# Optimization experiments

Hardware: AMD Instinct MI355X
Metric: run time of the kernel (lower is better)

## Reference

```python
import jax, jax.numpy as jnp
import numpy as np

T, D, H, P, HEADS, EC = 16, 192, 128, 128, 4, 32  # EC = proj_dim // 4
HD = P // HEADS  # head dim = 32


def setup_inputs() -> dict:
    key = jax.random.key(0)
    ks = jax.random.split(key, 16)
    def nrm(k, shp, s=0.02):
        return jax.random.normal(k, shp, jnp.float32) * s
    x = jax.random.normal(ks[0], (T, H, D), jnp.float32)
    u = jax.random.uniform(ks[1], (D, D))
    w = jax.random.uniform(ks[2], (D, D))
    edge_w = jnp.where(u < 0.05, w, 0.0)
    return dict(
        x=x, edge_w=edge_w,
        W_node=nrm(ks[3], (H, P)), b_node=jnp.zeros(P),
        W_edge=nrm(ks[4], (1, EC)), b_edge=jnp.zeros(EC),
        time_enc=nrm(ks[5], (P,)),
        Wqkv=nrm(ks[6], (P, 3 * P)), bqkv=jnp.zeros(3 * P),
        Wo=nrm(ks[7], (P, P)), bo=jnp.zeros(P),
        W1=nrm(ks[8], (P, 4 * P)), b1=jnp.zeros(4 * P),
        W2=nrm(ks[9], (4 * P, P)), b2=jnp.zeros(P),
        g1=jnp.ones(P), beta1=jnp.zeros(P), g2=jnp.ones(P), beta2=jnp.zeros(P),
        Wc1=nrm(ks[10], (2 * P + EC, P)), bc1=jnp.zeros(P),
        Wc2=nrm(ks[11], (P, 1)), bc2=jnp.zeros(1),
        Wd1=nrm(ks[12], (2 * P, P)), bd1=jnp.zeros(P),
        Wd2=nrm(ks[13], (P, 1)), bd2=jnp.zeros(1),
    )


def _ln(z, g, b):
    m = z.mean(-1, keepdims=True)
    v = ((z - m) ** 2).mean(-1, keepdims=True)
    return (z - m) / jnp.sqrt(v + 1e-5) * g + b


def _heads(t, S):
    return t.reshape(S, HEADS, HD).transpose(1, 0, 2)  # (h, S, hd)


def _forward(x, edge_w, W_node, b_node, W_edge, b_edge, time_enc, Wqkv, bqkv,
             Wo, bo, W1, b1, W2, b2, g1, beta1, g2, beta2,
             Wc1, bc1, Wc2, bc2, Wd1, bd1, Wd2, bd2):
    S = T * D
    # node encoder: (T,H,D) -> (T,D,H) -> (T*D,H) -> (T*D,P), dropout is eval-mode identity
    xf = x.transpose(0, 2, 1).reshape(S, H)
    h = jax.nn.relu(xf @ W_node + b_node)
    # learned time encoding scaled by time index
    t_idx = jnp.repeat(jnp.arange(T, dtype=jnp.float32), D)
    h = h + time_enc[None, :] * t_idx[:, None]
    # spatiotemporal mask: attend to self+neighbors at t and t-1 (vectorized kron)
    adj = (edge_w > 0) | jnp.eye(D, dtype=bool)
    time_allow = jnp.eye(T, dtype=bool) | jnp.eye(T, k=-1, dtype=bool)
    allow = (time_allow[:, None, :, None] & adj[None, :, None, :]).reshape(S, S)
    scale = 1.0 / np.sqrt(HD)
    z = h
    for _ in range(2):  # num_layers=2, shared weights as in the source
        y = _ln(z, g1, beta1)
        qkv = y @ Wqkv + bqkv
        q, k, v = jnp.split(qkv, 3, axis=-1)
        scores = jnp.einsum('hqd,hkd->hqk', _heads(q, S), _heads(k, S)) * scale
        scores = jnp.where(allow[None], scores, -jnp.inf)
        a = jax.nn.softmax(scores, axis=-1)
        attn = jnp.einsum('hqk,hkd->hqd', a, _heads(v, S))
        z = z + attn.transpose(1, 0, 2).reshape(S, P) @ Wo + bo
        y = _ln(z, g2, beta2)
        z = z + jax.nn.relu(y @ W1 + b1) @ W2 + b2
    nf = z.reshape(T, D, P)
    curr, nxt = nf[:-1], nf[1:]  # (T-1, D, P)
    # edge encoder: Linear(1->EC)+ReLU on edge weights
    edge_enc = jax.nn.relu(edge_w[:, :, None] * W_edge[0] + b_edge)  # (D, D, EC)
    # update classifier on concat[next_i, curr_j, edge] -> split the first matmul
    hn = nxt @ Wc1[:P]            # (T-1, D, P)
    hc = curr @ Wc1[P:2 * P]      # (T-1, D, P)
    he = edge_enc @ Wc1[2 * P:]   # (D, D, P)
    hcls = jax.nn.relu(hn[:, :, None, :] + hc[:, None, :, :] + he[None] + bc1)
    logits = (hcls @ Wc2)[..., 0] + bc2[0]  # (T-1, D, D)
    mask = (edge_w == 0) & ~jnp.eye(D, dtype=bool)
    logits = jnp.where(mask[None], -1e9, logits)
    # distance predictor on concat[curr, next]
    hd = jax.nn.relu(curr @ Wd1[:P] + nxt @ Wd1[P:] + bd1)
    dist = (hd @ Wd2)[..., 0] + bd2[0]  # (T-1, D)
    return logits, dist


def reference(x, edge_w, W_node, b_node, W_edge, b_edge, time_enc, Wqkv, bqkv,
              Wo, bo, W1, b1, W2, b2, g1, beta1, g2, beta2,
              Wc1, bc1, Wc2, bc2, Wd1, bd1, Wd2, bd2):
    return _forward(x, edge_w, W_node, b_node, W_edge, b_edge, time_enc, Wqkv,
                    bqkv, Wo, bo, W1, b1, W2, b2, g1, beta1, g2, beta2,
                    Wc1, bc1, Wc2, bc2, Wd1, bd1, Wd2, bd2)
```

## Files before the change

kernel.cpp:

```cpp
#include <hip/hip_runtime.h>

constexpr int T_ = 16;
constexpr int D_ = 192;
constexpr int H_ = 128;
constexpr int P_ = 128;
constexpr int EC_ = 32;
constexpr int S_ = T_ * D_;
constexpr int FF_ = 512;
constexpr float SCALE_ = 0.17677669529663687f;

__device__ __forceinline__ float wave_sum64(float v) {
#pragma unroll
  for (int m = 1; m < 64; m <<= 1) v += __shfl_xor(v, m);
  return v;
}

__global__ __launch_bounds__(128) void embed_adj_kernel(
    const float* __restrict__ x, const float* __restrict__ W_node,
    const float* __restrict__ b_node, const float* __restrict__ time_enc,
    const float* __restrict__ edge_w, float* __restrict__ z,
    int* __restrict__ adj_cnt, int* __restrict__ adj_list) {
  int bx = blockIdx.x;
  int tid = threadIdx.x;
  if (bx < D_ && tid < 64) {
    int lane = tid, cnt = 0;
    for (int base = 0; base < D_; base += 64) {
      int j = base + lane;
      bool pred = (edge_w[bx * D_ + j] > 0.f) || (j == bx);
      unsigned long long mb = __ballot(pred);
      int ofs = __popcll(mb & ((1ull << lane) - 1ull));
      if (pred) adj_list[bx * D_ + cnt + ofs] = j;
      cnt += __popcll(mb);
    }
    if (lane == 0) adj_cnt[bx] = cnt;
  }
  __shared__ float As[8 * H_];
  int m0 = bx * 8;
  for (int idx = tid; idx < 8 * H_; idx += 128) {
    int r = idx >> 7, h = idx & 127;
    int s = m0 + r, t = s / D_, d = s - t * D_;
    As[idx] = x[(t * H_ + h) * D_ + d];
  }
  __syncthreads();
  int j = tid;
  float acc[8];
  float bj = b_node[j];
#pragma unroll
  for (int r = 0; r < 8; ++r) acc[r] = bj;
  for (int h = 0; h < H_; h += 4) {
    float w0 = W_node[(h + 0) * P_ + j], w1 = W_node[(h + 1) * P_ + j];
    float w2 = W_node[(h + 2) * P_ + j], w3 = W_node[(h + 3) * P_ + j];
#pragma unroll
    for (int r = 0; r < 8; ++r) {
      const float4 a = *reinterpret_cast<const float4*>(&As[r * H_ + h]);
      acc[r] = fmaf(a.x, w0, acc[r]);
      acc[r] = fmaf(a.y, w1, acc[r]);
      acc[r] = fmaf(a.z, w2, acc[r]);
      acc[r] = fmaf(a.w, w3, acc[r]);
    }
  }
  float te = time_enc[j];
#pragma unroll
  for (int r = 0; r < 8; ++r) {
    int s = m0 + r;
    z[(size_t)s * P_ + j] = fmaxf(acc[r], 0.f) + te * (float)(s / D_);
  }
}

__global__ __launch_bounds__(192) void qkv_kernel(
    const float* __restrict__ z, const float* __restrict__ Wqkv,
    const float* __restrict__ bqkv, const float* __restrict__ g,
    const float* __restrict__ b, float* __restrict__ qkvb) {
  constexpr int BM = 16, NT = 192, N = 384;
  int m0 = blockIdx.x * BM;
  int tid = threadIdx.x;
  __shared__ float As[BM * 128];
  {
    float4* As4 = (float4*)As;
    const float4* Z4 = (const float4*)(z + (size_t)m0 * 128);
    for (int idx = tid; idx < BM * 32; idx += NT) As4[idx] = Z4[idx];
  }
  __syncthreads();
  {
    int wv = tid >> 6, lane = tid & 63;
    for (int r = wv; r < BM; r += 3) {
      float v0 = As[r * 128 + lane], v1 = As[r * 128 + 64 + lane];
      float s = wave_sum64(v0 + v1);
      float mean = s * (1.f / 128.f);
      float d0 = v0 - mean, d1 = v1 - mean;
      float q = wave_sum64(d0 * d0 + d1 * d1);
      float inv = 1.f / sqrtf(q * (1.f / 128.f) + 1e-5f);
      As[r * 128 + lane] = d0 * inv * g[lane] + b[lane];
      As[r * 128 + 64 + lane] = d1 * inv * g[lane + 64] + b[lane + 64];
    }
  }
  __syncthreads();
  int c0 = 2 * tid;
  float acc0[BM], acc1[BM];
  float b0c = bqkv[c0], b1c = bqkv[c0 + 1];
#pragma unroll
  for (int r = 0; r < BM; ++r) {
    acc0[r] = b0c;
    acc1[r] = b1c;
  }
  for (int k = 0; k < 128; k += 4) {
    float2 bv0 = *(const float2*)(Wqkv + (size_t)(k + 0) * N + c0);
    float2 bv1 = *(const float2*)(Wqkv + (size_t)(k + 1) * N + c0);
    float2 bv2 = *(const float2*)(Wqkv + (size_t)(k + 2) * N + c0);
    float2 bv3 = *(const float2*)(Wqkv + (size_t)(k + 3) * N + c0);
#pragma unroll
    for (int r = 0; r < BM; ++r) {
      const float4 a = *(const float4*)&As[r * 128 + k];
      acc0[r] = fmaf(a.x, bv0.x, acc0[r]);
      acc1[r] = fmaf(a.x, bv0.y, acc1[r]);
      acc0[r] = fmaf(a.y, bv1.x, acc0[r]);
      acc1[r] = fmaf(a.y, bv1.y, acc1[r]);
      acc0[r] = fmaf(a.z, bv2.x, acc0[r]);
      acc1[r] = fmaf(a.z, bv2.y, acc1[r]);
      acc0[r] = fmaf(a.w, bv3.x, acc0[r]);
      acc1[r] = fmaf(a.w, bv3.y, acc1[r]);
    }
  }
#pragma unroll
  for (int r = 0; r < BM; ++r) {
    float2 nv;
    nv.x = acc0[r];
    nv.y = acc1[r];
    *(float2*)(qkvb + (size_t)(m0 + r) * N + c0) = nv;
  }
}

__global__ __launch_bounds__(128) void attn_wo_kernel(
    const float* __restrict__ qkvb, const int* __restrict__ adj_cnt,
    const int* __restrict__ adj_list, const float* __restrict__ Wo,
    const float* __restrict__ bo, float* __restrict__ z) {
  int s = blockIdx.x;
  int t = s / D_, d1 = s - t * D_;
  int tid = threadIdx.x;
  __shared__ int klist[D_];
  __shared__ float scores[4][2 * D_];
  __shared__ float att[128];

  int nd2 = adj_cnt[d1];
  for (int kd = tid; kd < nd2; kd += 128) klist[kd] = adj_list[d1 * D_ + kd];
  __syncthreads();
  int t0 = (t > 0) ? t - 1 : 0;
  int ntp = (t > 0) ? 2 : 1;
  int nk = nd2 * ntp;

  float q = qkvb[(size_t)s * 384 + tid];
  int h = tid >> 5, dd = tid & 31;

  for (int tp = 0; tp < ntp; ++tp) {
    int tt = t0 + tp;
    for (int kd = 0; kd < nd2; ++kd) {
      int sk = tt * D_ + klist[kd];
      float partial = q * qkvb[(size_t)sk * 384 + P_ + tid];
      partial += __shfl_xor(partial, 1);
      partial += __shfl_xor(partial, 2);
      partial += __shfl_xor(partial, 4);
      partial += __shfl_xor(partial, 8);
      partial += __shfl_xor(partial, 16);
      if (dd == 0) scores[h][tp * nd2 + kd] = partial * SCALE_;
    }
  }
  float mx = -1e30f;
  for (int ki = dd; ki < nk; ki += 32) mx = fmaxf(mx, scores[h][ki]);
  mx = fmaxf(mx, __shfl_xor(mx, 1));
  mx = fmaxf(mx, __shfl_xor(mx, 2));
  mx = fmaxf(mx, __shfl_xor(mx, 4));
  mx = fmaxf(mx, __shfl_xor(mx, 8));
  mx = fmaxf(mx, __shfl_xor(mx, 16));
  float ssum = 0.f;
  for (int ki = dd; ki < nk; ki += 32) {
    float e = expf(scores[h][ki] - mx);
    scores[h][ki] = e;
    ssum += e;
  }
  ssum += __shfl_xor(ssum, 1);
  ssum += __shfl_xor(ssum, 2);
  ssum += __shfl_xor(ssum, 4);
  ssum += __shfl_xor(ssum, 8);
  ssum += __shfl_xor(ssum, 16);
  float inv = 1.f / ssum;

  float acc = 0.f;
  for (int tp = 0; tp < ntp; ++tp) {
    int tt = t0 + tp;
    for (int kd = 0; kd < nd2; ++kd) {
      float aev = scores[h][tp * nd2 + kd];
      int sk = tt * D_ + klist[kd];
      acc = fmaf(aev, qkvb[(size_t)sk * 384 + 2 * P_ + tid], acc);
    }
  }
  att[tid] = acc * inv;
  __syncthreads();

  int c = tid;
  float p = 0.f;
  for (int k = 0; k < 128; k += 4) {
    const float4 a = *(const float4*)&att[k];
    p = fmaf(a.x, Wo[(size_t)(k + 0) * P_ + c], p);
    p = fmaf(a.y, Wo[(size_t)(k + 1) * P_ + c], p);
    p = fmaf(a.z, Wo[(size_t)(k + 2) * P_ + c], p);
    p = fmaf(a.w, Wo[(size_t)(k + 3) * P_ + c], p);
  }
  z[(size_t)s * P_ + c] += p + bo[c];
}

__global__ __launch_bounds__(256) void ffn_kernel(
    const float* __restrict__ zin, const float* __restrict__ W1,
    const float* __restrict__ b1, const float* __restrict__ W2,
    const float* __restrict__ b2, const float* __restrict__ g,
    const float* __restrict__ b, float* __restrict__ z) {
  constexpr int BM = 8, NT = 256;
  int m0 = blockIdx.x * BM;
  int tid = threadIdx.x;
  __shared__ float As[BM * 128];
  __shared__ float mid[BM * FF_];
  {
    float4* As4 = (float4*)As;
    const float4* Z4 = (const float4*)(zin + (size_t)m0 * 128);
    for (int idx = tid; idx < BM * 32; idx += NT) As4[idx] = Z4[idx];
  }
  __syncthreads();
  {
    int wv = tid >> 6, lane = tid & 63;
    for (int r = wv; r < BM; r += 4) {
      float v0 = As[r * 128 + lane], v1 = As[r * 128 + 64 + lane];
      float s = wave_sum64(v0 + v1);
      float mean = s * (1.f / 128.f);
      float d0 = v0 - mean, d1 = v1 - mean;
      float qv = wave_sum64(d0 * d0 + d1 * d1);
      float inv = 1.f / sqrtf(qv * (1.f / 128.f) + 1e-5f);
      As[r * 128 + lane] = d0 * inv * g[lane] + b[lane];
      As[r * 128 + 64 + lane] = d1 * inv * g[lane + 64] + b[lane + 64];
    }
  }
  __syncthreads();
  {
    int c0 = 2 * tid;
    float acc0[BM], acc1[BM];
    float bb0 = b1[c0], bb1 = b1[c0 + 1];
#pragma unroll
    for (int r = 0; r < BM; ++r) {
      acc0[r] = bb0;
      acc1[r] = bb1;
    }
    for (int k = 0; k < 128; k += 4) {
      float2 bv0 = *(const float2*)(W1 + (size_t)(k + 0) * FF_ + c0);
      float2 bv1 = *(const float2*)(W1 + (size_t)(k + 1) * FF_ + c0);
      float2 bv2 = *(const float2*)(W1 + (size_t)(k + 2) * FF_ + c0);
      float2 bv3 = *(const float2*)(W1 + (size_t)(k + 3) * FF_ + c0);
#pragma unroll
      for (int r = 0; r < BM; ++r) {
        const float4 a = *(const float4*)&As[r * 128 + k];
        acc0[r] = fmaf(a.x, bv0.x, acc0[r]);
        acc1[r] = fmaf(a.x, bv0.y, acc1[r]);
        acc0[r] = fmaf(a.y, bv1.x, acc0[r]);
        acc1[r] = fmaf(a.y, bv1.y, acc1[r]);
        acc0[r] = fmaf(a.z, bv2.x, acc0[r]);
        acc1[r] = fmaf(a.z, bv2.y, acc1[r]);
        acc0[r] = fmaf(a.w, bv3.x, acc0[r]);
        acc1[r] = fmaf(a.w, bv3.y, acc1[r]);
      }
    }
#pragma unroll
    for (int r = 0; r < BM; ++r) {
      mid[r * FF_ + c0] = fmaxf(acc0[r], 0.f);
      mid[r * FF_ + c0 + 1] = fmaxf(acc1[r], 0.f);
    }
  }
  __syncthreads();
  {
    int rg = tid >> 7, col = tid & 127;
    int r0 = rg * 4;
    float acc[4] = {0.f, 0.f, 0.f, 0.f};
    for (int k = 0; k < FF_; k += 4) {
      float w0 = W2[(size_t)(k + 0) * P_ + col];
      float w1 = W2[(size_t)(k + 1) * P_ + col];
      float w2 = W2[(size_t)(k + 2) * P_ + col];
      float w3 = W2[(size_t)(k + 3) * P_ + col];
#pragma unroll
      for (int i = 0; i < 4; ++i) {
        const float4 a = *(const float4*)&mid[(r0 + i) * FF_ + k];
        acc[i] = fmaf(a.x, w0, acc[i]);
        acc[i] = fmaf(a.y, w1, acc[i]);
        acc[i] = fmaf(a.z, w2, acc[i]);
        acc[i] = fmaf(a.w, w3, acc[i]);
      }
    }
    float bb = b2[col];
#pragma unroll
    for (int i = 0; i < 4; ++i)
      z[(size_t)(m0 + r0 + i) * P_ + col] += acc[i] + bb;
  }
}

__global__ __launch_bounds__(256) void pre_gemm_kernel(
    const float* __restrict__ A, const float* __restrict__ Wc1,
    const float* __restrict__ Wd1, float* __restrict__ pre) {
  constexpr int K = 128, N = 512, NT = 256, BM = 8;
  int m0 = blockIdx.x * BM;
  int tid = threadIdx.x;
  __shared__ float As[BM * K];
  {
    float4* As4 = (float4*)As;
    const float4* A4 = (const float4*)(A + (size_t)m0 * K);
    for (int idx = tid; idx < BM * K / 4; idx += NT) As4[idx] = A4[idx];
  }
  __syncthreads();
  int c0 = 2 * tid;
  int seg = c0 >> 7, cc = c0 & 127;
  const float* Bbase = (seg < 2 ? Wc1 : Wd1) + ((seg & 1) ? P_ * P_ : 0) + cc;
  float acc0[BM], acc1[BM];
#pragma unroll
  for (int r = 0; r < BM; ++r) {
    acc0[r] = 0.f;
    acc1[r] = 0.f;
  }
  for (int k = 0; k < K; k += 4) {
    float2 bv0 = *(const float2*)(Bbase + (size_t)(k + 0) * P_);
    float2 bv1 = *(const float2*)(Bbase + (size_t)(k + 1) * P_);
    float2 bv2 = *(const float2*)(Bbase + (size_t)(k + 2) * P_);
    float2 bv3 = *(const float2*)(Bbase + (size_t)(k + 3) * P_);
#pragma unroll
    for (int r = 0; r < BM; ++r) {
      const float4 a = *(const float4*)&As[r * K + k];
      acc0[r] = fmaf(a.x, bv0.x, acc0[r]);
      acc1[r] = fmaf(a.x, bv0.y, acc1[r]);
      acc0[r] = fmaf(a.y, bv1.x, acc0[r]);
      acc1[r] = fmaf(a.y, bv1.y, acc1[r]);
      acc0[r] = fmaf(a.z, bv2.x, acc0[r]);
      acc1[r] = fmaf(a.z, bv2.y, acc1[r]);
      acc0[r] = fmaf(a.w, bv3.x, acc0[r]);
      acc1[r] = fmaf(a.w, bv3.y, acc1[r]);
    }
  }
#pragma unroll
  for (int r = 0; r < BM; ++r) {
    float2 nv;
    nv.x = acc0[r];
    nv.y = acc1[r];
    *(float2*)(pre + (size_t)(m0 + r) * N + c0) = nv;
  }
}

__global__ __launch_bounds__(64) void logits_dist_kernel(
    const float* __restrict__ pre, const int* __restrict__ adj_cnt,
    const int* __restrict__ adj_list, const float* __restrict__ edge_w,
    const float* __restrict__ W_edge, const float* __restrict__ b_edge,
    const float* __restrict__ Wc1e, const float* __restrict__ bc1,
    const float* __restrict__ Wc2, const float* __restrict__ bc2,
    const float* __restrict__ bd1, const float* __restrict__ Wd2,
    const float* __restrict__ bd2, float* __restrict__ logits,
    float* __restrict__ dist) {
  int i = blockIdx.x;
  int t = blockIdx.y;
  int lane = threadIdx.x;
  int w = t * D_ + i;
  float* lrow = logits + (size_t)w * D_;
  for (int j = lane; j < D_; j += 64) lrow[j] = -1e9f;

  const float* hnr = pre + (size_t)((t + 1) * D_ + i) * 512;
  float hn0 = hnr[lane], hn1 = hnr[lane + 64];
  float bc1_0 = bc1[lane], bc1_1 = bc1[lane + 64];
  float wc0 = Wc2[lane], wc1 = Wc2[lane + 64];
  float bb = bc2[0];
  int cnt = adj_cnt[i];
  for (int jj = 0; jj < cnt; ++jj) {
    int j = adj_list[i * D_ + jj];
    float wv = edge_w[i * D_ + j];
    float he0 = 0.f, he1 = 0.f;
#pragma unroll 8
    for (int e = 0; e < EC_; ++e) {
      float enc = fmaxf(fmaf(wv, W_edge[e], b_edge[e]), 0.f);
      he0 = fmaf(enc, Wc1e[e * P_ + lane], he0);
      he1 = fmaf(enc, Wc1e[e * P_ + lane + 64], he1);
    }
    const float* hcr = pre + (size_t)(t * D_ + j) * 512 + 128;
    float sacc = fmaxf(hn0 + hcr[lane] + he0 + bc1_0, 0.f) * wc0 +
                 fmaxf(hn1 + hcr[lane + 64] + he1 + bc1_1, 0.f) * wc1;
    sacc = wave_sum64(sacc);
    if (lane == 0) lrow[j] = sacc + bb;
  }

  const float* ar = pre + (size_t)w * 512 + 256;
  const float* br = pre + (size_t)(w + D_) * 512 + 384;
  float v0 = fmaxf(ar[lane] + br[lane] + bd1[lane], 0.f) * Wd2[lane];
  float v1 = fmaxf(ar[lane + 64] + br[lane + 64] + bd1[lane + 64], 0.f) * Wd2[lane + 64];
  float sd = wave_sum64(v0 + v1);
  if (lane == 0) dist[w] = sd + bd2[0];
}

extern "C" void kernel_launch(void* const* d_in, const int* in_sizes, int n_in,
                              void* d_out, int out_size, void* d_ws,
                              size_t ws_size, hipStream_t stream) {
  const float* x = (const float*)d_in[0];
  const float* edge_w = (const float*)d_in[1];
  const float* W_node = (const float*)d_in[2];
  const float* b_node = (const float*)d_in[3];
  const float* W_edge = (const float*)d_in[4];
  const float* b_edge = (const float*)d_in[5];
  const float* time_enc = (const float*)d_in[6];
  const float* Wqkv = (const float*)d_in[7];
  const float* bqkv = (const float*)d_in[8];
  const float* Wo = (const float*)d_in[9];
  const float* bo = (const float*)d_in[10];
  const float* W1 = (const float*)d_in[11];
  const float* b1 = (const float*)d_in[12];
  const float* W2 = (const float*)d_in[13];
  const float* b2 = (const float*)d_in[14];
  const float* g1 = (const float*)d_in[15];
  const float* beta1 = (const float*)d_in[16];
  const float* g2 = (const float*)d_in[17];
  const float* beta2 = (const float*)d_in[18];
  const float* Wc1 = (const float*)d_in[19];
  const float* bc1 = (const float*)d_in[20];
  const float* Wc2 = (const float*)d_in[21];
  const float* bc2 = (const float*)d_in[22];
  const float* Wd1 = (const float*)d_in[23];
  const float* bd1 = (const float*)d_in[24];
  const float* Wd2 = (const float*)d_in[25];
  const float* bd2 = (const float*)d_in[26];

  float* ws = (float*)d_ws;
  float* z = ws;
  float* qkvb = z + S_ * 128;
  float* pre = qkvb + S_ * 384;
  int* adj_cnt = (int*)(pre + S_ * 512);
  int* adj_list = adj_cnt + D_;

  float* logits = (float*)d_out;
  float* dist = (float*)d_out + (T_ - 1) * D_ * D_;

  embed_adj_kernel<<<S_ / 8, 128, 0, stream>>>(x, W_node, b_node, time_enc,
                                               edge_w, z, adj_cnt, adj_list);
  for (int it = 0; it < 2; ++it) {
    qkv_kernel<<<S_ / 16, 192, 0, stream>>>(z, Wqkv, bqkv, g1, beta1, qkvb);
    attn_wo_kernel<<<S_, 128, 0, stream>>>(qkvb, adj_cnt, adj_list, Wo, bo, z);
    ffn_kernel<<<S_ / 8, 256, 0, stream>>>(z, W1, b1, W2, b2, g2, beta2, z);
  }
  pre_gemm_kernel<<<S_ / 8, 256, 0, stream>>>(z, Wc1, Wd1, pre);
  logits_dist_kernel<<<dim3(D_, T_ - 1), 64, 0, stream>>>(
      pre, adj_cnt, adj_list, edge_w, W_edge, b_edge, Wc1 + 2 * P_ * P_, bc1,
      Wc2, bc2, bd1, Wd2, bd2, logits, dist);
}
```

Baseline: 326.1 us.

## Fuse attention, output projection and FFN into one tail kernel; widen GEMM blocks

Merges the per-row attention+Wo kernel and the FFN kernel into a single 512-thread tail kernel. Each block handles 8 rows: four 128-thread groups compute attention for two rows each, then the Wo projection, LayerNorm, and both FFN GEMMs run on data kept in shared memory. This removes one launch per layer and a global round-trip of z. The qkv and pre-GEMM kernels are also reshaped to one output column per thread with more threads and fewer rows per block. In exchange, the attention part now runs fewer blocks with extra barriers, and the smaller row tiles reuse each weight load less.

```diff
diff --git a/kernel.cpp b/kernel.cpp
--- a/kernel.cpp
+++ b/kernel.cpp
@@ -67,23 +67,23 @@
   }
 }
 
-__global__ __launch_bounds__(192) void qkv_kernel(
+__global__ __launch_bounds__(384) void qkv_kernel(
     const float* __restrict__ z, const float* __restrict__ Wqkv,
     const float* __restrict__ bqkv, const float* __restrict__ g,
     const float* __restrict__ b, float* __restrict__ qkvb) {
-  constexpr int BM = 16, NT = 192, N = 384;
+  constexpr int BM = 8, N = 384;
   int m0 = blockIdx.x * BM;
   int tid = threadIdx.x;
   __shared__ float As[BM * 128];
   {
     float4* As4 = (float4*)As;
     const float4* Z4 = (const float4*)(z + (size_t)m0 * 128);
-    for (int idx = tid; idx < BM * 32; idx += NT) As4[idx] = Z4[idx];
+    if (tid < 256) As4[tid] = Z4[tid];
   }
   __syncthreads();
   {
     int wv = tid >> 6, lane = tid & 63;
-    for (int r = wv; r < BM; r += 3) {
+    for (int r = wv; r < BM; r += 6) {
       float v0 = As[r * 128 + lane], v1 = As[r * 128 + 64 + lane];
       float s = wave_sum64(v0 + v1);
       float mean = s * (1.f / 128.f);
@@ -95,255 +95,226 @@
     }
   }
   __syncthreads();
-  int c0 = 2 * tid;
-  float acc0[BM], acc1[BM];
-  float b0c = bqkv[c0], b1c = bqkv[c0 + 1];
-#pragma unroll
-  for (int r = 0; r < BM; ++r) {
-    acc0[r] = b0c;
-    acc1[r] = b1c;
-  }
+  int col = tid;
+  float acc[BM];
+  float bc = bqkv[col];
+#pragma unroll
+  for (int r = 0; r < BM; ++r) acc[r] = bc;
   for (int k = 0; k < 128; k += 4) {
-    float2 bv0 = *(const float2*)(Wqkv + (size_t)(k + 0) * N + c0);
-    float2 bv1 = *(const float2*)(Wqkv + (size_t)(k + 1) * N + c0);
-    float2 bv2 = *(const float2*)(Wqkv + (size_t)(k + 2) * N + c0);
-    float2 bv3 = *(const float2*)(Wqkv + (size_t)(k + 3) * N + c0);
+    float b0 = Wqkv[(size_t)(k + 0) * N + col];
+    float b1 = Wqkv[(size_t)(k + 1) * N + col];
+    float b2 = Wqkv[(size_t)(k + 2) * N + col];
+    float b3 = Wqkv[(size_t)(k + 3) * N + col];
 #pragma unroll
     for (int r = 0; r < BM; ++r) {
       const float4 a = *(const float4*)&As[r * 128 + k];
-      acc0[r] = fmaf(a.x, bv0.x, acc0[r]);
-      acc1[r] = fmaf(a.x, bv0.y, acc1[r]);
-      acc0[r] = fmaf(a.y, bv1.x, acc0[r]);
-      acc1[r] = fmaf(a.y, bv1.y, acc1[r]);
-      acc0[r] = fmaf(a.z, bv2.x, acc0[r]);
-      acc1[r] = fmaf(a.z, bv2.y, acc1[r]);
-      acc0[r] = fmaf(a.w, bv3.x, acc0[r]);
-      acc1[r] = fmaf(a.w, bv3.y, acc1[r]);
-    }
-  }
-#pragma unroll
-  for (int r = 0; r < BM; ++r) {
-    float2 nv;
-    nv.x = acc0[r];
-    nv.y = acc1[r];
-    *(float2*)(qkvb + (size_t)(m0 + r) * N + c0) = nv;
-  }
-}
-
-__global__ __launch_bounds__(128) void attn_wo_kernel(
+      acc[r] = fmaf(a.x, b0, acc[r]);
+      acc[r] = fmaf(a.y, b1, acc[r]);
+      acc[r] = fmaf(a.z, b2, acc[r]);
+      acc[r] = fmaf(a.w, b3, acc[r]);
+    }
+  }
+#pragma unroll
+  for (int r = 0; r < BM; ++r) qkvb[(size_t)(m0 + r) * N + col] = acc[r];
+}
+
+__global__ __launch_bounds__(512) void tail_kernel(
     const float* __restrict__ qkvb, const int* __restrict__ adj_cnt,
     const int* __restrict__ adj_list, const float* __restrict__ Wo,
-    const float* __restrict__ bo, float* __restrict__ z) {
-  int s = blockIdx.x;
-  int t = s / D_, d1 = s - t * D_;
-  int tid = threadIdx.x;
-  __shared__ int klist[D_];
-  __shared__ float scores[4][2 * D_];
-  __shared__ float att[128];
-
-  int nd2 = adj_cnt[d1];
-  for (int kd = tid; kd < nd2; kd += 128) klist[kd] = adj_list[d1 * D_ + kd];
-  __syncthreads();
-  int t0 = (t > 0) ? t - 1 : 0;
-  int ntp = (t > 0) ? 2 : 1;
-  int nk = nd2 * ntp;
-
-  float q = qkvb[(size_t)s * 384 + tid];
-  int h = tid >> 5, dd = tid & 31;
-
-  for (int tp = 0; tp < ntp; ++tp) {
-    int tt = t0 + tp;
-    for (int kd = 0; kd < nd2; ++kd) {
-      int sk = tt * D_ + klist[kd];
-      float partial = q * qkvb[(size_t)sk * 384 + P_ + tid];
-      partial += __shfl_xor(partial, 1);
-      partial += __shfl_xor(partial, 2);
-      partial += __shfl_xor(partial, 4);
-      partial += __shfl_xor(partial, 8);
-      partial += __shfl_xor(partial, 16);
-      if (dd == 0) scores[h][tp * nd2 + kd] = partial * SCALE_;
-    }
-  }
-  float mx = -1e30f;
-  for (int ki = dd; ki < nk; ki += 32) mx = fmaxf(mx, scores[h][ki]);
-  mx = fmaxf(mx, __shfl_xor(mx, 1));
-  mx = fmaxf(mx, __shfl_xor(mx, 2));
-  mx = fmaxf(mx, __shfl_xor(mx, 4));
-  mx = fmaxf(mx, __shfl_xor(mx, 8));
-  mx = fmaxf(mx, __shfl_xor(mx, 16));
-  float ssum = 0.f;
-  for (int ki = dd; ki < nk; ki += 32) {
-    float e = expf(scores[h][ki] - mx);
-    scores[h][ki] = e;
-    ssum += e;
-  }
-  ssum += __shfl_xor(ssum, 1);
-  ssum += __shfl_xor(ssum, 2);
-  ssum += __shfl_xor(ssum, 4);
-  ssum += __shfl_xor(ssum, 8);
-  ssum += __shfl_xor(ssum, 16);
-  float inv = 1.f / ssum;
-
-  float acc = 0.f;
-  for (int tp = 0; tp < ntp; ++tp) {
-    int tt = t0 + tp;
-    for (int kd = 0; kd < nd2; ++kd) {
-      float aev = scores[h][tp * nd2 + kd];
-      int sk = tt * D_ + klist[kd];
-      acc = fmaf(aev, qkvb[(size_t)sk * 384 + 2 * P_ + tid], acc);
-    }
-  }
-  att[tid] = acc * inv;
-  __syncthreads();
-
-  int c = tid;
-  float p = 0.f;
-  for (int k = 0; k < 128; k += 4) {
-    const float4 a = *(const float4*)&att[k];
-    p = fmaf(a.x, Wo[(size_t)(k + 0) * P_ + c], p);
-    p = fmaf(a.y, Wo[(size_t)(k + 1) * P_ + c], p);
-    p = fmaf(a.z, Wo[(size_t)(k + 2) * P_ + c], p);
-    p = fmaf(a.w, Wo[(size_t)(k + 3) * P_ + c], p);
-  }
-  z[(size_t)s * P_ + c] += p + bo[c];
-}
-
-__global__ __launch_bounds__(256) void ffn_kernel(
-    const float* __restrict__ zin, const float* __restrict__ W1,
+    const float* __restrict__ bo, const float* __restrict__ W1,
     const float* __restrict__ b1, const float* __restrict__ W2,
-    const float* __restrict__ b2, const float* __restrict__ g,
-    const float* __restrict__ b, float* __restrict__ z) {
-  constexpr int BM = 8, NT = 256;
+    const float* __restrict__ b2, const float* __restrict__ g2,
+    const float* __restrict__ beta2, float* __restrict__ z) {
+  constexpr int BM = 8;
   int m0 = blockIdx.x * BM;
   int tid = threadIdx.x;
-  __shared__ float As[BM * 128];
-  __shared__ float mid[BM * FF_];
-  {
-    float4* As4 = (float4*)As;
-    const float4* Z4 = (const float4*)(zin + (size_t)m0 * 128);
-    for (int idx = tid; idx < BM * 32; idx += NT) As4[idx] = Z4[idx];
-  }
-  __syncthreads();
+  __shared__ float att[BM][128];
+  __shared__ float zs[BM][128];
+  __shared__ __align__(16) unsigned char uA[32768];
+
+  {
+    int gq = tid >> 7, lt = tid & 127;
+    int h = lt >> 5, dd = lt & 31;
+    int* klist = (int*)(uA + gq * 8192);
+    float* scores = (float*)(uA + gq * 8192 + 768);
+    for (int qi = 0; qi < 2; ++qi) {
+      int r = gq * 2 + qi;
+      int s = m0 + r;
+      int t = s / D_, d1 = s - t * D_;
+      int nd2 = adj_cnt[d1];
+      __syncthreads();
+      for (int kd = lt; kd < nd2; kd += 128) klist[kd] = adj_list[d1 * D_ + kd];
+      __syncthreads();
+      int t0 = (t > 0) ? t - 1 : 0;
+      int ntp = (t > 0) ? 2 : 1;
+      int nk = nd2 * ntp;
+      float q = qkvb[(size_t)s * 384 + lt];
+      for (int tp = 0; tp < ntp; ++tp) {
+        int tt = t0 + tp;
+        for (int kd = 0; kd < nd2; ++kd) {
+          int sk = tt * D_ + klist[kd];
+          float partial = q * qkvb[(size_t)sk * 384 + P_ + lt];
+          partial += __shfl_xor(partial, 1);
+          partial += __shfl_xor(partial, 2);
+          partial += __shfl_xor(partial, 4);
+          partial += __shfl_xor(partial, 8);
+          partial += __shfl_xor(partial, 16);
+          if (dd == 0) scores[h * 384 + tp * nd2 + kd] = partial * SCALE_;
+        }
+      }
+      float mx = -1e30f;
+      for (int ki = dd; ki < nk; ki += 32) mx = fmaxf(mx, scores[h * 384 + ki]);
+      mx = fmaxf(mx, __shfl_xor(mx, 1));
+      mx = fmaxf(mx, __shfl_xor(mx, 2));
+      mx = fmaxf(mx, __shfl_xor(mx, 4));
+      mx = fmaxf(mx, __shfl_xor(mx, 8));
+      mx = fmaxf(mx, __shfl_xor(mx, 16));
+      float ssum = 0.f;
+      for (int ki = dd; ki < nk; ki += 32) {
+        float e = expf(scores[h * 384 + ki] - mx);
+        scores[h * 384 + ki] = e;
+        ssum += e;
+      }
+      ssum += __shfl_xor(ssum, 1);
+      ssum += __shfl_xor(ssum, 2);
+      ssum += __shfl_xor(ssum, 4);
+      ssum += __shfl_xor(ssum, 8);
+      ssum += __shfl_xor(ssum, 16);
+      float inv = 1.f / ssum;
+      float acc = 0.f;
+      for (int tp = 0; tp < ntp; ++tp) {
+        int tt = t0 + tp;
+        for (int kd = 0; kd < nd2; ++kd) {
+          float aev = scores[h * 384 + tp * nd2 + kd];
+          int sk = tt * D_ + klist[kd];
+          acc = fmaf(aev, qkvb[(size_t)sk * 384 + 2 * P_ + lt], acc);
+        }
+      }
+      att[r][lt] = acc * inv;
+    }
+  }
+  __syncthreads();
+
+  {
+    int col = tid & 127, rg = tid >> 7;
+    int r0 = rg * 2;
+    float p0 = 0.f, p1 = 0.f;
+    for (int k = 0; k < 128; k += 4) {
+      float w0 = Wo[(size_t)(k + 0) * P_ + col];
+      float w1 = Wo[(size_t)(k + 1) * P_ + col];
+      float w2 = Wo[(size_t)(k + 2) * P_ + col];
+      float w3 = Wo[(size_t)(k + 3) * P_ + col];
+      const float4 a0 = *(const float4*)&att[r0][k];
+      const float4 a1 = *(const float4*)&att[r0 + 1][k];
+      p0 = fmaf(a0.x, w0, p0); p0 = fmaf(a0.y, w1, p0);
+      p0 = fmaf(a0.z, w2, p0); p0 = fmaf(a0.w, w3, p0);
+      p1 = fmaf(a1.x, w0, p1); p1 = fmaf(a1.y, w1, p1);
+      p1 = fmaf(a1.z, w2, p1); p1 = fmaf(a1.w, w3, p1);
+    }
+    float bb = bo[col];
+    zs[r0][col] = z[(size_t)(m0 + r0) * P_ + col] + p0 + bb;
+    zs[r0 + 1][col] = z[(size_t)(m0 + r0 + 1) * P_ + col] + p1 + bb;
+  }
+  __syncthreads();
+
+  float* mid = (float*)uA;
+  float* ys = (float*)(uA + 16384);
+
   {
     int wv = tid >> 6, lane = tid & 63;
-    for (int r = wv; r < BM; r += 4) {
-      float v0 = As[r * 128 + lane], v1 = As[r * 128 + 64 + lane];
-      float s = wave_sum64(v0 + v1);
-      float mean = s * (1.f / 128.f);
-      float d0 = v0 - mean, d1 = v1 - mean;
-      float qv = wave_sum64(d0 * d0 + d1 * d1);
-      float inv = 1.f / sqrtf(qv * (1.f / 128.f) + 1e-5f);
-      As[r * 128 + lane] = d0 * inv * g[lane] + b[lane];
-      As[r * 128 + 64 + lane] = d1 * inv * g[lane + 64] + b[lane + 64];
-    }
-  }
-  __syncthreads();
-  {
-    int c0 = 2 * tid;
-    float acc0[BM], acc1[BM];
-    float bb0 = b1[c0], bb1 = b1[c0 + 1];
-#pragma unroll
-    for (int r = 0; r < BM; ++r) {
-      acc0[r] = bb0;
-      acc1[r] = bb1;
-    }
+    float v0 = zs[wv][lane], v1 = zs[wv][lane + 64];
+    float ssm = wave_sum64(v0 + v1);
+    float mean = ssm * (1.f / 128.f);
+    float d0 = v0 - mean, d1 = v1 - mean;
+    float qv = wave_sum64(d0 * d0 + d1 * d1);
+    float inv = 1.f / sqrtf(qv * (1.f / 128.f) + 1e-5f);
+    ys[wv * 128 + lane] = d0 * inv * g2[lane] + beta2[lane];
+    ys[wv * 128 + lane + 64] = d1 * inv * g2[lane + 64] + beta2[lane + 64];
+  }
+  __syncthreads();
+
+  {
+    int col = tid;
+    float acc[8];
+    float bb = b1[col];
+#pragma unroll
+    for (int r = 0; r < 8; ++r) acc[r] = bb;
     for (int k = 0; k < 128; k += 4) {
-      float2 bv0 = *(const float2*)(W1 + (size_t)(k + 0) * FF_ + c0);
-      float2 bv1 = *(const float2*)(W1 + (size_t)(k + 1) * FF_ + c0);
-      float2 bv2 = *(const float2*)(W1 + (size_t)(k + 2) * FF_ + c0);
-      float2 bv3 = *(const float2*)(W1 + (size_t)(k + 3) * FF_ + c0);
-#pragma unroll
-      for (int r = 0; r < BM; ++r) {
-        const float4 a = *(const float4*)&As[r * 128 + k];
-        acc0[r] = fmaf(a.x, bv0.x, acc0[r]);
-        acc1[r] = fmaf(a.x, bv0.y, acc1[r]);
-        acc0[r] = fmaf(a.y, bv1.x, acc0[r]);
-        acc1[r] = fmaf(a.y, bv1.y, acc1[r]);
-        acc0[r] = fmaf(a.z, bv2.x, acc0[r]);
-        acc1[r] = fmaf(a.z, bv2.y, acc1[r]);
-        acc0[r] = fmaf(a.w, bv3.x, acc0[r]);
-        acc1[r] = fmaf(a.w, bv3.y, acc1[r]);
+      float w0 = W1[(size_t)(k + 0) * FF_ + col];
+      float w1 = W1[(size_t)(k + 1) * FF_ + col];
+      float w2 = W1[(size_t)(k + 2) * FF_ + col];
+      float w3 = W1[(size_t)(k + 3) * FF_ + col];
+#pragma unroll
+      for (int r = 0; r < 8; ++r) {
+        const float4 a = *(const float4*)&ys[r * 128 + k];
+        acc[r] = fmaf(a.x, w0, acc[r]);
+        acc[r] = fmaf(a.y, w1, acc[r]);
+        acc[r] = fmaf(a.z, w2, acc[r]);
+        acc[r] = fmaf(a.w, w3, acc[r]);
       }
     }
 #pragma unroll
-    for (int r = 0; r < BM; ++r) {
-      mid[r * FF_ + c0] = fmaxf(acc0[r], 0.f);
-      mid[r * FF_ + c0 + 1] = fmaxf(acc1[r], 0.f);
-    }
-  }
-  __syncthreads();
-  {
-    int rg = tid >> 7, col = tid & 127;
-    int r0 = rg * 4;
-    float acc[4] = {0.f, 0.f, 0.f, 0.f};
+    for (int r = 0; r < 8; ++r) mid[r * FF_ + col] = fmaxf(acc[r], 0.f);
+  }
+  __syncthreads();
+
+  {
+    int col = tid & 127, rg = tid >> 7;
+    int r0 = rg * 2;
+    float a0 = 0.f, a1 = 0.f;
     for (int k = 0; k < FF_; k += 4) {
       float w0 = W2[(size_t)(k + 0) * P_ + col];
       float w1 = W2[(size_t)(k + 1) * P_ + col];
       float w2 = W2[(size_t)(k + 2) * P_ + col];
       float w3 = W2[(size_t)(k + 3) * P_ + col];
-#pragma unroll
-      for (int i = 0; i < 4; ++i) {
-        const float4 a = *(const float4*)&mid[(r0 + i) * FF_ + k];
-        acc[i] = fmaf(a.x, w0, acc[i]);
-        acc[i] = fmaf(a.y, w1, acc[i]);
-        acc[i] = fmaf(a.z, w2, acc[i]);
-        acc[i] = fmaf(a.w, w3, acc[i]);
-      }
+      const float4 m0v = *(const float4*)&mid[r0 * FF_ + k];
+      const float4 m1v = *(const float4*)&mid[(r0 + 1) * FF_ + k];
+      a0 = fmaf(m0v.x, w0, a0); a0 = fmaf(m0v.y, w1, a0);
+      a0 = fmaf(m0v.z, w2, a0); a0 = fmaf(m0v.w, w3, a0);
+      a1 = fmaf(m1v.x, w0, a1); a1 = fmaf(m1v.y, w1, a1);
+      a1 = fmaf(m1v.z, w2, a1); a1 = fmaf(m1v.w, w3, a1);
     }
     float bb = b2[col];
-#pragma unroll
-    for (int i = 0; i < 4; ++i)
-      z[(size_t)(m0 + r0 + i) * P_ + col] += acc[i] + bb;
-  }
-}
-
-__global__ __launch_bounds__(256) void pre_gemm_kernel(
+    z[(size_t)(m0 + r0) * P_ + col] = zs[r0][col] + a0 + bb;
+    z[(size_t)(m0 + r0 + 1) * P_ + col] = zs[r0 + 1][col] + a1 + bb;
+  }
+}
+
+__global__ __launch_bounds__(512) void pre_gemm_kernel(
     const float* __restrict__ A, const float* __restrict__ Wc1,
     const float* __restrict__ Wd1, float* __restrict__ pre) {
-  constexpr int K = 128, N = 512, NT = 256, BM = 8;
+  constexpr int K = 128, BM = 8;
   int m0 = blockIdx.x * BM;
   int tid = threadIdx.x;
   __shared__ float As[BM * K];
   {
     float4* As4 = (float4*)As;
     const float4* A4 = (const float4*)(A + (size_t)m0 * K);
-    for (int idx = tid; idx < BM * K / 4; idx += NT) As4[idx] = A4[idx];
-  }
-  __syncthreads();
-  int c0 = 2 * tid;
-  int seg = c0 >> 7, cc = c0 & 127;
+    if (tid < 256) As4[tid] = A4[tid];
+  }
+  __syncthreads();
+  int col = tid;
+  int seg = col >> 7, cc = col & 127;
   const float* Bbase = (seg < 2 ? Wc1 : Wd1) + ((seg & 1) ? P_ * P_ : 0) + cc;
-  float acc0[BM], acc1[BM];
-#pragma unroll
-  for (int r = 0; r < BM; ++r) {
-    acc0[r] = 0.f;
-    acc1[r] = 0.f;
-  }
+  float acc[BM];
+#pragma unroll
+  for (int r = 0; r < BM; ++r) acc[r] = 0.f;
   for (int k = 0; k < K; k += 4) {
-    float2 bv0 = *(const float2*)(Bbase + (size_t)(k + 0) * P_);
-    float2 bv1 = *(const float2*)(Bbase + (size_t)(k + 1) * P_);
-    float2 bv2 = *(const float2*)(Bbase + (size_t)(k + 2) * P_);
-    float2 bv3 = *(const float2*)(Bbase + (size_t)(k + 3) * P_);
+    float b0 = Bbase[(size_t)(k + 0) * P_];
+    float b1 = Bbase[(size_t)(k + 1) * P_];
+    float b2 = Bbase[(size_t)(k + 2) * P_];
+    float b3 = Bbase[(size_t)(k + 3) * P_];
 #pragma unroll
     for (int r = 0; r < BM; ++r) {
       const float4 a = *(const float4*)&As[r * K + k];
-      acc0[r] = fmaf(a.x, bv0.x, acc0[r]);
-      acc1[r] = fmaf(a.x, bv0.y, acc1[r]);
-      acc0[r] = fmaf(a.y, bv1.x, acc0[r]);
-      acc1[r] = fmaf(a.y, bv1.y, acc1[r]);
-      acc0[r] = fmaf(a.z, bv2.x, acc0[r]);
-      acc1[r] = fmaf(a.z, bv2.y, acc1[r]);
-      acc0[r] = fmaf(a.w, bv3.x, acc0[r]);
-      acc1[r] = fmaf(a.w, bv3.y, acc1[r]);
-    }
-  }
-#pragma unroll
-  for (int r = 0; r < BM; ++r) {
-    float2 nv;
-    nv.x = acc0[r];
-    nv.y = acc1[r];
-    *(float2*)(pre + (size_t)(m0 + r) * N + c0) = nv;
-  }
+      acc[r] = fmaf(a.x, b0, acc[r]);
+      acc[r] = fmaf(a.y, b1, acc[r]);
+      acc[r] = fmaf(a.z, b2, acc[r]);
+      acc[r] = fmaf(a.w, b3, acc[r]);
+    }
+  }
+#pragma unroll
+  for (int r = 0; r < BM; ++r) pre[(size_t)(m0 + r) * 512 + col] = acc[r];
 }
 
 __global__ __launch_bounds__(64) void logits_dist_kernel(
@@ -437,11 +408,11 @@
   embed_adj_kernel<<<S_ / 8, 128, 0, stream>>>(x, W_node, b_node, time_enc,
                                                edge_w, z, adj_cnt, adj_list);
   for (int it = 0; it < 2; ++it) {
-    qkv_kernel<<<S_ / 16, 192, 0, stream>>>(z, Wqkv, bqkv, g1, beta1, qkvb);
-    attn_wo_kernel<<<S_, 128, 0, stream>>>(qkvb, adj_cnt, adj_list, Wo, bo, z);
-    ffn_kernel<<<S_ / 8, 256, 0, stream>>>(z, W1, b1, W2, b2, g2, beta2, z);
-  }
-  pre_gemm_kernel<<<S_ / 8, 256, 0, stream>>>(z, Wc1, Wd1, pre);
+    qkv_kernel<<<S_ / 8, 384, 0, stream>>>(z, Wqkv, bqkv, g1, beta1, qkvb);
+    tail_kernel<<<S_ / 8, 512, 0, stream>>>(qkvb, adj_cnt, adj_list, Wo, bo,
+                                            W1, b1, W2, b2, g2, beta2, z);
+  }
+  pre_gemm_kernel<<<S_ / 8, 512, 0, stream>>>(z, Wc1, Wd1, pre);
   logits_dist_kernel<<<dim3(D_, T_ - 1), 64, 0, stream>>>(
       pre, adj_cnt, adj_list, edge_w, W_edge, b_edge, Wc1 + 2 * P_ * P_, bc1,
       Wc2, bc2, bd1, Wd2, bd2, logits, dist);
```

After: 334.5 us. +2.6%, slower.

## Shrink GEMM row tiles, widen blocks, and unroll attention key loops by two

Applied to the files above, without the earlier changes.

The row tiles of the embed, qkv and ffn kernels shrink to 4 rows. The qkv and pre_gemm kernels switch to one output column per thread, with 384 and 512 threads per block. This launches more and wider blocks so the compute units fill up better on the small problem, at the cost of loading each weight from global memory more times. The attention score and value loops are also unrolled by two, so independent loads and shuffle reductions can overlap and hide latency.

```diff
diff --git a/kernel.cpp b/kernel.cpp
--- a/kernel.cpp
+++ b/kernel.cpp
@@ -34,24 +34,24 @@
     }
     if (lane == 0) adj_cnt[bx] = cnt;
   }
-  __shared__ float As[8 * H_];
-  int m0 = bx * 8;
-  for (int idx = tid; idx < 8 * H_; idx += 128) {
+  __shared__ float As[4 * H_];
+  int m0 = bx * 4;
+  for (int idx = tid; idx < 4 * H_; idx += 128) {
     int r = idx >> 7, h = idx & 127;
     int s = m0 + r, t = s / D_, d = s - t * D_;
     As[idx] = x[(t * H_ + h) * D_ + d];
   }
   __syncthreads();
   int j = tid;
-  float acc[8];
+  float acc[4];
   float bj = b_node[j];
 #pragma unroll
-  for (int r = 0; r < 8; ++r) acc[r] = bj;
+  for (int r = 0; r < 4; ++r) acc[r] = bj;
   for (int h = 0; h < H_; h += 4) {
     float w0 = W_node[(h + 0) * P_ + j], w1 = W_node[(h + 1) * P_ + j];
     float w2 = W_node[(h + 2) * P_ + j], w3 = W_node[(h + 3) * P_ + j];
 #pragma unroll
-    for (int r = 0; r < 8; ++r) {
+    for (int r = 0; r < 4; ++r) {
       const float4 a = *reinterpret_cast<const float4*>(&As[r * H_ + h]);
       acc[r] = fmaf(a.x, w0, acc[r]);
       acc[r] = fmaf(a.y, w1, acc[r]);
@@ -61,29 +61,30 @@
   }
   float te = time_enc[j];
 #pragma unroll
-  for (int r = 0; r < 8; ++r) {
+  for (int r = 0; r < 4; ++r) {
     int s = m0 + r;
     z[(size_t)s * P_ + j] = fmaxf(acc[r], 0.f) + te * (float)(s / D_);
   }
 }
 
-__global__ __launch_bounds__(192) void qkv_kernel(
+__global__ __launch_bounds__(384) void qkv_kernel(
     const float* __restrict__ z, const float* __restrict__ Wqkv,
     const float* __restrict__ bqkv, const float* __restrict__ g,
     const float* __restrict__ b, float* __restrict__ qkvb) {
-  constexpr int BM = 16, NT = 192, N = 384;
+  constexpr int BM = 4, N = 384;
   int m0 = blockIdx.x * BM;
   int tid = threadIdx.x;
   __shared__ float As[BM * 128];
   {
     float4* As4 = (float4*)As;
     const float4* Z4 = (const float4*)(z + (size_t)m0 * 128);
-    for (int idx = tid; idx < BM * 32; idx += NT) As4[idx] = Z4[idx];
+    if (tid < BM * 32) As4[tid] = Z4[tid];
   }
   __syncthreads();
   {
     int wv = tid >> 6, lane = tid & 63;
-    for (int r = wv; r < BM; r += 3) {
+    if (wv < BM) {
+      int r = wv;
       float v0 = As[r * 128 + lane], v1 = As[r * 128 + 64 + lane];
       float s = wave_sum64(v0 + v1);
       float mean = s * (1.f / 128.f);
@@ -95,39 +96,27 @@
     }
   }
   __syncthreads();
-  int c0 = 2 * tid;
-  float acc0[BM], acc1[BM];
-  float b0c = bqkv[c0], b1c = bqkv[c0 + 1];
-#pragma unroll
-  for (int r = 0; r < BM; ++r) {
-    acc0[r] = b0c;
-    acc1[r] = b1c;
-  }
+  int col = tid;
+  float acc[BM];
+  float bc = bqkv[col];
+#pragma unroll
+  for (int r = 0; r < BM; ++r) acc[r] = bc;
   for (int k = 0; k < 128; k += 4) {
-    float2 bv0 = *(const float2*)(Wqkv + (size_t)(k + 0) * N + c0);
-    float2 bv1 = *(const float2*)(Wqkv + (size_t)(k + 1) * N + c0);
-    float2 bv2 = *(const float2*)(Wqkv + (size_t)(k + 2) * N + c0);
-    float2 bv3 = *(const float2*)(Wqkv + (size_t)(k + 3) * N + c0);
+    float b0 = Wqkv[(size_t)(k + 0) * N + col];
+    float b1 = Wqkv[(size_t)(k + 1) * N + col];
+    float b2 = Wqkv[(size_t)(k + 2) * N + col];
+    float b3 = Wqkv[(size_t)(k + 3) * N + col];
 #pragma unroll
     for (int r = 0; r < BM; ++r) {
       const float4 a = *(const float4*)&As[r * 128 + k];
-      acc0[r] = fmaf(a.x, bv0.x, acc0[r]);
-      acc1[r] = fmaf(a.x, bv0.y, acc1[r]);
-      acc0[r] = fmaf(a.y, bv1.x, acc0[r]);
-      acc1[r] = fmaf(a.y, bv1.y, acc1[r]);
-      acc0[r] = fmaf(a.z, bv2.x, acc0[r]);
-      acc1[r] = fmaf(a.z, bv2.y, acc1[r]);
-      acc0[r] = fmaf(a.w, bv3.x, acc0[r]);
-      acc1[r] = fmaf(a.w, bv3.y, acc1[r]);
-    }
-  }
-#pragma unroll
-  for (int r = 0; r < BM; ++r) {
-    float2 nv;
-    nv.x = acc0[r];
-    nv.y = acc1[r];
-    *(float2*)(qkvb + (size_t)(m0 + r) * N + c0) = nv;
-  }
+      acc[r] = fmaf(a.x, b0, acc[r]);
+      acc[r] = fmaf(a.y, b1, acc[r]);
+      acc[r] = fmaf(a.z, b2, acc[r]);
+      acc[r] = fmaf(a.w, b3, acc[r]);
+    }
+  }
+#pragma unroll
+  for (int r = 0; r < BM; ++r) qkvb[(size_t)(m0 + r) * N + col] = acc[r];
 }
 
 __global__ __launch_bounds__(128) void attn_wo_kernel(
@@ -153,44 +142,62 @@
 
   for (int tp = 0; tp < ntp; ++tp) {
     int tt = t0 + tp;
-    for (int kd = 0; kd < nd2; ++kd) {
+    int kd = 0;
+    for (; kd + 2 <= nd2; kd += 2) {
+      int sk0 = tt * D_ + klist[kd];
+      int sk1 = tt * D_ + klist[kd + 1];
+      float p0 = q * qkvb[(size_t)sk0 * 384 + P_ + tid];
+      float p1 = q * qkvb[(size_t)sk1 * 384 + P_ + tid];
+#pragma unroll
+      for (int m = 1; m < 32; m <<= 1) {
+        p0 += __shfl_xor(p0, m);
+        p1 += __shfl_xor(p1, m);
+      }
+      if (dd == 0) {
+        scores[h][tp * nd2 + kd] = p0 * SCALE_;
+        scores[h][tp * nd2 + kd + 1] = p1 * SCALE_;
+      }
+    }
+    if (kd < nd2) {
       int sk = tt * D_ + klist[kd];
-      float partial = q * qkvb[(size_t)sk * 384 + P_ + tid];
-      partial += __shfl_xor(partial, 1);
-      partial += __shfl_xor(partial, 2);
-      partial += __shfl_xor(partial, 4);
-      partial += __shfl_xor(partial, 8);
-      partial += __shfl_xor(partial, 16);
-      if (dd == 0) scores[h][tp * nd2 + kd] = partial * SCALE_;
+      float p = q * qkvb[(size_t)sk * 384 + P_ + tid];
+#pragma unroll
+      for (int m = 1; m < 32; m <<= 1) p += __shfl_xor(p, m);
+      if (dd == 0) scores[h][tp * nd2 + kd] = p * SCALE_;
     }
   }
   float mx = -1e30f;
   for (int ki = dd; ki < nk; ki += 32) mx = fmaxf(mx, scores[h][ki]);
-  mx = fmaxf(mx, __shfl_xor(mx, 1));
-  mx = fmaxf(mx, __shfl_xor(mx, 2));
-  mx = fmaxf(mx, __shfl_xor(mx, 4));
-  mx = fmaxf(mx, __shfl_xor(mx, 8));
-  mx = fmaxf(mx, __shfl_xor(mx, 16));
+#pragma unroll
+  for (int m = 1; m < 32; m <<= 1) mx = fmaxf(mx, __shfl_xor(mx, m));
   float ssum = 0.f;
   for (int ki = dd; ki < nk; ki += 32) {
     float e = expf(scores[h][ki] - mx);
     scores[h][ki] = e;
     ssum += e;
   }
-  ssum += __shfl_xor(ssum, 1);
-  ssum += __shfl_xor(ssum, 2);
-  ssum += __shfl_xor(ssum, 4);
-  ssum += __shfl_xor(ssum, 8);
-  ssum += __shfl_xor(ssum, 16);
+#pragma unroll
+  for (int m = 1; m < 32; m <<= 1) ssum += __shfl_xor(ssum, m);
   float inv = 1.f / ssum;
 
   float acc = 0.f;
   for (int tp = 0; tp < ntp; ++tp) {
     int tt = t0 + tp;
-    for (int kd = 0; kd < nd2; ++kd) {
-      float aev = scores[h][tp * nd2 + kd];
+    int kd = 0;
+    for (; kd + 2 <= nd2; kd += 2) {
+      float e0 = scores[h][tp * nd2 + kd];
+      float e1 = scores[h][tp * nd2 + kd + 1];
+      int sk0 = tt * D_ + klist[kd];
+      int sk1 = tt * D_ + klist[kd + 1];
+      float v0 = qkvb[(size_t)sk0 * 384 + 2 * P_ + tid];
+      float v1 = qkvb[(size_t)sk1 * 384 + 2 * P_ + tid];
+      acc = fmaf(e0, v0, acc);
+      acc = fmaf(e1, v1, acc);
+    }
+    if (kd < nd2) {
+      float e = scores[h][tp * nd2 + kd];
       int sk = tt * D_ + klist[kd];
-      acc = fmaf(aev, qkvb[(size_t)sk * 384 + 2 * P_ + tid], acc);
+      acc = fmaf(e, qkvb[(size_t)sk * 384 + 2 * P_ + tid], acc);
     }
   }
   att[tid] = acc * inv;
@@ -209,33 +216,31 @@
 }
 
 __global__ __launch_bounds__(256) void ffn_kernel(
-    const float* __restrict__ zin, const float* __restrict__ W1,
-    const float* __restrict__ b1, const float* __restrict__ W2,
-    const float* __restrict__ b2, const float* __restrict__ g,
-    const float* __restrict__ b, float* __restrict__ z) {
-  constexpr int BM = 8, NT = 256;
+    const float* __restrict__ W1, const float* __restrict__ b1,
+    const float* __restrict__ W2, const float* __restrict__ b2,
+    const float* __restrict__ g, const float* __restrict__ b,
+    float* __restrict__ z) {
+  constexpr int BM = 4, NT = 256;
   int m0 = blockIdx.x * BM;
   int tid = threadIdx.x;
   __shared__ float As[BM * 128];
   __shared__ float mid[BM * FF_];
   {
     float4* As4 = (float4*)As;
-    const float4* Z4 = (const float4*)(zin + (size_t)m0 * 128);
-    for (int idx = tid; idx < BM * 32; idx += NT) As4[idx] = Z4[idx];
+    const float4* Z4 = (const float4*)(z + (size_t)m0 * 128);
+    if (tid < BM * 32) As4[tid] = Z4[tid];
   }
   __syncthreads();
   {
     int wv = tid >> 6, lane = tid & 63;
-    for (int r = wv; r < BM; r += 4) {
-      float v0 = As[r * 128 + lane], v1 = As[r * 128 + 64 + lane];
-      float s = wave_sum64(v0 + v1);
-      float mean = s * (1.f / 128.f);
-      float d0 = v0 - mean, d1 = v1 - mean;
-      float qv = wave_sum64(d0 * d0 + d1 * d1);
-      float inv = 1.f / sqrtf(qv * (1.f / 128.f) + 1e-5f);
-      As[r * 128 + lane] = d0 * inv * g[lane] + b[lane];
-      As[r * 128 + 64 + lane] = d1 * inv * g[lane + 64] + b[lane + 64];
-    }
+    float v0 = As[wv * 128 + lane], v1 = As[wv * 128 + 64 + lane];
+    float s = wave_sum64(v0 + v1);
+    float mean = s * (1.f / 128.f);
+    float d0 = v0 - mean, d1 = v1 - mean;
+    float qv = wave_sum64(d0 * d0 + d1 * d1);
+    float inv = 1.f / sqrtf(qv * (1.f / 128.f) + 1e-5f);
+    As[wv * 128 + lane] = d0 * inv * g[lane] + b[lane];
+    As[wv * 128 + lane + 64] = d1 * inv * g[lane + 64] + b[lane + 64];
   }
   __syncthreads();
   {
@@ -274,76 +279,61 @@
   __syncthreads();
   {
     int rg = tid >> 7, col = tid & 127;
-    int r0 = rg * 4;
-    float acc[4] = {0.f, 0.f, 0.f, 0.f};
+    int r0 = rg * 2;
+    float a0 = 0.f, a1 = 0.f;
     for (int k = 0; k < FF_; k += 4) {
       float w0 = W2[(size_t)(k + 0) * P_ + col];
       float w1 = W2[(size_t)(k + 1) * P_ + col];
       float w2 = W2[(size_t)(k + 2) * P_ + col];
       float w3 = W2[(size_t)(k + 3) * P_ + col];
-#pragma unroll
-      for (int i = 0; i < 4; ++i) {
-        const float4 a = *(const float4*)&mid[(r0 + i) * FF_ + k];
-        acc[i] = fmaf(a.x, w0, acc[i]);
-        acc[i] = fmaf(a.y, w1, acc[i]);
-        acc[i] = fmaf(a.z, w2, acc[i]);
-        acc[i] = fmaf(a.w, w3, acc[i]);
-      }
+      const float4 m0v = *(const float4*)&mid[r0 * FF_ + k];
+      const float4 m1v = *(const float4*)&mid[(r0 + 1) * FF_ + k];
+      a0 = fmaf(m0v.x, w0, a0); a0 = fmaf(m0v.y, w1, a0);
+      a0 = fmaf(m0v.z, w2, a0); a0 = fmaf(m0v.w, w3, a0);
+      a1 = fmaf(m1v.x, w0, a1); a1 = fmaf(m1v.y, w1, a1);
+      a1 = fmaf(m1v.z, w2, a1); a1 = fmaf(m1v.w, w3, a1);
     }
     float bb = b2[col];
-#pragma unroll
-    for (int i = 0; i < 4; ++i)
-      z[(size_t)(m0 + r0 + i) * P_ + col] += acc[i] + bb;
-  }
-}
-
-__global__ __launch_bounds__(256) void pre_gemm_kernel(
+    z[(size_t)(m0 + r0) * P_ + col] += a0 + bb;
+    z[(size_t)(m0 + r0 + 1) * P_ + col] += a1 + bb;
+  }
+}
+
+__global__ __launch_bounds__(512) void pre_gemm_kernel(
     const float* __restrict__ A, const float* __restrict__ Wc1,
     const float* __restrict__ Wd1, float* __restrict__ pre) {
-  constexpr int K = 128, N = 512, NT = 256, BM = 8;
+  constexpr int K = 128, BM = 8;
   int m0 = blockIdx.x * BM;
   int tid = threadIdx.x;
   __shared__ float As[BM * K];
   {
     float4* As4 = (float4*)As;
     const float4* A4 = (const float4*)(A + (size_t)m0 * K);
-    for (int idx = tid; idx < BM * K / 4; idx += NT) As4[idx] = A4[idx];
-  }
-  __syncthreads();
-  int c0 = 2 * tid;
-  int seg = c0 >> 7, cc = c0 & 127;
+    if (tid < 256) As4[tid] = A4[tid];
+  }
+  __syncthreads();
+  int col = tid;
+  int seg = col >> 7, cc = col & 127;
   const float* Bbase = (seg < 2 ? Wc1 : Wd1) + ((seg & 1) ? P_ * P_ : 0) + cc;
-  float acc0[BM], acc1[BM];
-#pragma unroll
-  for (int r = 0; r < BM; ++r) {
-    acc0[r] = 0.f;
-    acc1[r] = 0.f;
-  }
+  float acc[BM];
+#pragma unroll
+  for (int r = 0; r < BM; ++r) acc[r] = 0.f;
   for (int k = 0; k < K; k += 4) {
-    float2 bv0 = *(const float2*)(Bbase + (size_t)(k + 0) * P_);
-    float2 bv1 = *(const float2*)(Bbase + (size_t)(k + 1) * P_);
-    float2 bv2 = *(const float2*)(Bbase + (size_t)(k + 2) * P_);
-    float2 bv3 = *(const float2*)(Bbase + (size_t)(k + 3) * P_);
+    float b0 = Bbase[(size_t)(k + 0) * P_];
+    float b1 = Bbase[(size_t)(k + 1) * P_];
+    float b2 = Bbase[(size_t)(k + 2) * P_];
+    float b3 = Bbase[(size_t)(k + 3) * P_];
 #pragma unroll
     for (int r = 0; r < BM; ++r) {
       const float4 a = *(const float4*)&As[r * K + k];
-      acc0[r] = fmaf(a.x, bv0.x, acc0[r]);
-      acc1[r] = fmaf(a.x, bv0.y, acc1[r]);
-      acc0[r] = fmaf(a.y, bv1.x, acc0[r]);
-      acc1[r] = fmaf(a.y, bv1.y, acc1[r]);
-      acc0[r] = fmaf(a.z, bv2.x, acc0[r]);
-      acc1[r] = fmaf(a.z, bv2.y, acc1[r]);
-      acc0[r] = fmaf(a.w, bv3.x, acc0[r]);
-      acc1[r] = fmaf(a.w, bv3.y, acc1[r]);
-    }
-  }
-#pragma unroll
-  for (int r = 0; r < BM; ++r) {
-    float2 nv;
-    nv.x = acc0[r];
-    nv.y = acc1[r];
-    *(float2*)(pre + (size_t)(m0 + r) * N + c0) = nv;
-  }
+      acc[r] = fmaf(a.x, b0, acc[r]);
+      acc[r] = fmaf(a.y, b1, acc[r]);
+      acc[r] = fmaf(a.z, b2, acc[r]);
+      acc[r] = fmaf(a.w, b3, acc[r]);
+    }
+  }
+#pragma unroll
+  for (int r = 0; r < BM; ++r) pre[(size_t)(m0 + r) * 512 + col] = acc[r];
 }
 
 __global__ __launch_bounds__(64) void logits_dist_kernel(
@@ -434,14 +424,14 @@
   float* logits = (float*)d_out;
   float* dist = (float*)d_out + (T_ - 1) * D_ * D_;
 
-  embed_adj_kernel<<<S_ / 8, 128, 0, stream>>>(x, W_node, b_node, time_enc,
+  embed_adj_kernel<<<S_ / 4, 128, 0, stream>>>(x, W_node, b_node, time_enc,
                                                edge_w, z, adj_cnt, adj_list);
   for (int it = 0; it < 2; ++it) {
-    qkv_kernel<<<S_ / 16, 192, 0, stream>>>(z, Wqkv, bqkv, g1, beta1, qkvb);
+    qkv_kernel<<<S_ / 4, 384, 0, stream>>>(z, Wqkv, bqkv, g1, beta1, qkvb);
     attn_wo_kernel<<<S_, 128, 0, stream>>>(qkvb, adj_cnt, adj_list, Wo, bo, z);
-    ffn_kernel<<<S_ / 8, 256, 0, stream>>>(z, W1, b1, W2, b2, g2, beta2, z);
-  }
-  pre_gemm_kernel<<<S_ / 8, 256, 0, stream>>>(z, Wc1, Wd1, pre);
+    ffn_kernel<<<S_ / 4, 256, 0, stream>>>(W1, b1, W2, b2, g2, beta2, z);
+  }
+  pre_gemm_kernel<<<S_ / 8, 512, 0, stream>>>(z, Wc1, Wd1, pre);
   logits_dist_kernel<<<dim3(D_, T_ - 1), 64, 0, stream>>>(
       pre, adj_cnt, adj_list, edge_w, W_edge, b_edge, Wc1 + 2 * P_ * P_, bc1,
       Wc2, bc2, bd1, Wd2, bd2, logits, dist);
```

Result: faster. 295.4 us (-9.4%).
